# Performance work log

Hardware: AMD Instinct MI355X
Metric: run time of the kernel (lower is better)

Reference implementation:

```python
import jax, jax.numpy as jnp
import numpy as np

CHANNEL = 64
RATIO = 8
C1 = CHANNEL // RATIO


def setup_inputs() -> dict:
    key = jax.random.key(0)
    ks = jax.random.split(key, 8)
    b, c, h, w = 2, CHANNEL, 96, 96
    X = jax.random.normal(ks[0], (b, c, h, w), dtype=jnp.float32)
    Y = jax.random.normal(ks[1], (b, c, h, w), dtype=jnp.float32)
    # 1x1 conv weights (stored as [out, in]) + biases, Kaiming-ish scale
    s = 1.0 / np.sqrt(c)
    Wq = jax.random.uniform(ks[2], (C1, c), jnp.float32, -s, s)
    bq = jax.random.uniform(ks[3], (C1,), jnp.float32, -s, s)
    Wk = jax.random.uniform(ks[4], (C1, c), jnp.float32, -s, s)
    bk = jax.random.uniform(ks[5], (C1,), jnp.float32, -s, s)
    Wv = jax.random.uniform(ks[6], (c, c), jnp.float32, -s, s)
    bv = jax.random.uniform(ks[7], (c,), jnp.float32, -s, s)
    return {"X": X, "Y": Y, "Wq": Wq, "bq": bq, "Wk": Wk, "bk": bk, "Wv": Wv, "bv": bv}


def reference(X, Y, Wq, bq, Wk, bk, Wv, bv):
    b, c, h, w = Y.shape
    n = h * w
    # 1x1 convs as channel contractions -> [b, n, c_out]
    Xf = X.reshape(b, c, n)                       # [b, c, n]
    q = jnp.einsum('oc,bcn->bno', Wq, Xf) + bq    # [b, n, c1]
    k = jnp.einsum('oc,bcn->bno', Wk, Xf) + bk    # [b, n, c1]
    v = jnp.einsum('oc,bcn->bno', Wv, Y.reshape(b, c, n)) + bv  # [b, n, c]
    scores = jnp.einsum('bic,bjc->bij', q, k)     # [b, n, n]
    # NOTE: softmax over dim=1 (the first n axis), as in the original module
    a = jax.nn.softmax(scores, axis=1)
    x = jnp.einsum('bij,bjc->bic', a, v)          # [b, n, c]
    x = x.transpose(0, 2, 1).reshape(b, c, h, w)
    return Y + x
```

## Files before the change

### kernel.cpp

```cpp
#include <hip/hip_runtime.h>

#define NPOS 9216
#define NB 2
#define CCH 64
#define JSPLIT 8
#define JCHUNK (NPOS / JSPLIT)
#define NSTEP (JCHUNK / 64)

typedef __attribute__((ext_vector_type(8))) short short8;
typedef __attribute__((ext_vector_type(4))) short short4b;
typedef __attribute__((ext_vector_type(4))) float f32x4;
typedef __attribute__((ext_vector_type(16))) float f32x16;

#define LOG2E 1.4426950408889634f

__device__ __forceinline__ f32x4 mfma16(short4b a, short4b b, f32x4 c) {
#if defined(__HIP_DEVICE_COMPILE__)
    return __builtin_amdgcn_mfma_f32_16x16x16bf16_1k(a, b, c, 0, 0, 0);
#else
    return c;
#endif
}

__device__ __forceinline__ ushort f2bf(float x) {
    unsigned u = __builtin_bit_cast(unsigned, x);
    u += 0x7FFFu + ((u >> 16) & 1u);
    return (ushort)(u >> 16);
}

__device__ __forceinline__ unsigned cvt_pk_bf16(float lo, float hi) {
    unsigned r;
    asm("v_cvt_pk_bf16_f32 %0, %1, %2" : "=v"(r) : "v"(lo), "v"(hi));
    return r;
}

__global__ __launch_bounds__(256) void qkv_kernel(
    const float* __restrict__ X, const float* __restrict__ Y,
    const float* __restrict__ Wq, const float* __restrict__ bq,
    const float* __restrict__ Wk, const float* __restrict__ bk,
    const float* __restrict__ Wv, const float* __restrict__ bv,
    ushort* __restrict__ qb, ushort* __restrict__ kb,
    ushort* __restrict__ vT, float* __restrict__ out)
{
    __shared__ float wqkT[1024];
    __shared__ float wvTs[4096];
    int tid = threadIdx.x;
    for (int idx = tid; idx < 1024; idx += 256) {
        int c = idx >> 4, o = idx & 15;
        wqkT[idx] = (o < 8) ? Wq[o * 64 + c] : Wk[(o - 8) * 64 + c];
    }
    for (int idx = tid; idx < 4096; idx += 256) {
        int c = idx >> 6, o = idx & 63;
        wvTs[idx] = Wv[o * 64 + c];
    }
    __syncthreads();

    int p = tid & 31, s = tid >> 5;
    int base = blockIdx.x * 32;
    int b = base / NPOS;
    int n = (base % NPOS) + p;

    float va[8], qk[8], ysave[8];
    #pragma unroll
    for (int o = 0; o < 8; ++o) va[o] = bv[s * 8 + o];
    #pragma unroll
    for (int o = 0; o < 8; ++o) qk[o] = 0.f;
    if (s == 0) {
        #pragma unroll
        for (int o = 0; o < 8; ++o) qk[o] = bq[o];
    } else if (s == 1) {
        #pragma unroll
        for (int o = 0; o < 8; ++o) qk[o] = bk[o];
    }

    const float* Xb = X + (size_t)b * CCH * NPOS + n;
    const float* Yb = Y + (size_t)b * CCH * NPOS + n;
    for (int co = 0; co < 8; ++co) {
        #pragma unroll
        for (int ci = 0; ci < 8; ++ci) {
            int c = co * 8 + ci;
            float yv = Yb[(size_t)c * NPOS];
            if (co == s) ysave[ci] = yv;
            const float* wv = wvTs + c * 64 + s * 8;
            #pragma unroll
            for (int o = 0; o < 8; ++o) va[o] += wv[o] * yv;
            if (s < 2) {
                float xv = Xb[(size_t)c * NPOS];
                const float* wq = wqkT + c * 16 + s * 8;
                #pragma unroll
                for (int o = 0; o < 8; ++o) qk[o] += wq[o] * xv;
            }
        }
    }

    ushort* vdst = vT + (size_t)b * CCH * NPOS + n;
    float* ob = out + (size_t)b * CCH * NPOS + n;
    #pragma unroll
    for (int o = 0; o < 8; ++o) {
        vdst[(size_t)(s * 8 + o) * NPOS] = f2bf(va[o]);
        ob[(size_t)(s * 8 + o) * NPOS] = ysave[o];
    }
    if (s < 2) {
        if (s == 0) {
            #pragma unroll
            for (int o = 0; o < 8; ++o) qk[o] *= LOG2E;
        }
        short8 row;
        #pragma unroll
        for (int o = 0; o < 8; ++o) row[o] = (short)f2bf(qk[o]);
        ushort* dst = (s == 0 ? qb : kb) + ((size_t)b * NPOS + n) * 8;
        *(short8*)dst = row;
    }
}

__global__ __launch_bounds__(256) void zpass_kernel(
    const ushort* __restrict__ qb, const ushort* __restrict__ kb,
    float* __restrict__ Z)
{
    int tid = threadIdx.x;
    int w = tid >> 6, l = tid & 63;
    int il2 = l & 31, h = l >> 5;
    int b = blockIdx.z;
    int jb = blockIdx.x * 128 + w * 32;
    int i0 = blockIdx.y * 1152;
    const short8 zero8 = {0,0,0,0,0,0,0,0};
    f32x16 cz16;
    #pragma unroll
    for (int r = 0; r < 16; ++r) cz16[r] = 0.f;

    short8 kf = zero8;
    if (h == 0) kf = *(const short8*)(kb + ((size_t)b * NPOS + jb + il2) * 8);

    f32x16 za = cz16;
    const ushort* qrow = qb + ((size_t)b * NPOS + i0 + il2) * 8;
    short8 qf = (h == 0) ? *(const short8*)qrow : zero8;
    for (int it = 0; it < 36; ++it) {
        short8 qn = zero8;
        if (h == 0 && (it + 1) < 36)
            qn = *(const short8*)(qrow + (size_t)(it + 1) * 256);
        f32x16 sv = __builtin_amdgcn_mfma_f32_32x32x16_bf16(kf, qf, cz16, 0, 0, 0);
        #pragma unroll
        for (int r = 0; r < 16; ++r) za[r] += __builtin_amdgcn_exp2f(sv[r]);
        qf = qn;
    }
    #pragma unroll
    for (int r = 0; r < 16; ++r) {
        float x = za[r];
        x += __shfl_xor(x, 1, 32);
        x += __shfl_xor(x, 2, 32);
        x += __shfl_xor(x, 4, 32);
        x += __shfl_xor(x, 8, 32);
        x += __shfl_xor(x, 16, 32);
        za[r] = x;
    }
    if (il2 == 0) {
        #pragma unroll
        for (int r = 0; r < 16; ++r) {
            int j = jb + (r & 3) + 8 * (r >> 2) + 4 * h;
            atomicAdd(&Z[(size_t)b * NPOS + j], za[r]);
        }
    }
}

__global__ __launch_bounds__(256) void pass2_kernel(
    const ushort* __restrict__ qb, const ushort* __restrict__ kb,
    const ushort* __restrict__ vT, const float* __restrict__ Z,
    float* __restrict__ out)
{
    __shared__ ushort vz[2][64 * 64];
    int tid = threadIdx.x;
    int w = tid >> 6, l = tid & 63;
    int il = l & 15, g = l >> 4;
    int b = blockIdx.z;
    int ibase = blockIdx.x * 64;
    int j0 = blockIdx.y * JCHUNK;
    int jw = w * 16;

    const short8 zero8 = {0,0,0,0,0,0,0,0};
    const f32x4 cz = {0.f,0.f,0.f,0.f};

    short8 qf[4];
    #pragma unroll
    for (int it = 0; it < 4; ++it) {
        qf[it] = zero8;
        if (g == 0)
            qf[it] = *(const short8*)(qb + ((size_t)b * NPOS + ibase + it * 16 + il) * 8);
    }

    f32x4 acc[4][4];
    #pragma unroll
    for (int cg = 0; cg < 4; ++cg)
        #pragma unroll
        for (int it = 0; it < 4; ++it) acc[cg][it] = cz;

    const ushort* kbb = kb + (size_t)b * NPOS * 8;
    const float* Zb = Z + (size_t)b * NPOS;

    int sr = tid >> 2, sq = tid & 3;
    const ushort* vrow = vT + (size_t)b * CCH * NPOS + (size_t)sr * NPOS + j0;
    int so0 = (sq ^ (sr & 7)) * 8;
    int so1 = ((sq + 4) ^ (sr & 7)) * 8;

    {
        float4 ga = *(const float4*)(vrow + sq * 8);
        float4 gb = *(const float4*)(vrow + sq * 8 + 32);
        *(float4*)&vz[0][sr * 64 + so0] = ga;
        *(float4*)&vz[0][sr * 64 + so1] = gb;
    }
    short8 kf = zero8;
    if (g == 0) kf = *(const short8*)(kbb + (size_t)(j0 + jw + il) * 8);
    float4 Zv = *(const float4*)(Zb + j0 + jw + 4 * g);
    __syncthreads();

    int rslot = 2 * w + (g >> 1);
    int rbyte = (g & 1) * 4;

    for (int st = 0; st < NSTEP; ++st) {
        int cur = st & 1;
        bool more = (st + 1) < NSTEP;

        float4 ga = {0,0,0,0}, gb = {0,0,0,0}, Zn = {0,0,0,0};
        short8 kn = zero8;
        if (more) {
            int jn = (st + 1) * 64;
            ga = *(const float4*)(vrow + jn + sq * 8);
            gb = *(const float4*)(vrow + jn + sq * 8 + 32);
            if (g == 0) kn = *(const short8*)(kbb + (size_t)(j0 + jn + jw + il) * 8);
            Zn = *(const float4*)(Zb + j0 + jn + jw + 4 * g);
        }

        f32x4 sv[4];
        #pragma unroll
        for (int it = 0; it < 4; ++it)
            sv[it] = __builtin_amdgcn_mfma_f32_16x16x32_bf16(kf, qf[it], cz, 0, 0, 0);

        float r0 = __builtin_amdgcn_rcpf(Zv.x);
        float r1 = __builtin_amdgcn_rcpf(Zv.y);
        float r2 = __builtin_amdgcn_rcpf(Zv.z);
        float r3 = __builtin_amdgcn_rcpf(Zv.w);

        short4b pf[4];
        #pragma unroll
        for (int it = 0; it < 4; ++it) {
            float p0 = __builtin_amdgcn_exp2f(sv[it][0]) * r0;
            float p1 = __builtin_amdgcn_exp2f(sv[it][1]) * r1;
            float p2 = __builtin_amdgcn_exp2f(sv[it][2]) * r2;
            float p3 = __builtin_amdgcn_exp2f(sv[it][3]) * r3;
            uint2 u;
            u.x = cvt_pk_bf16(p0, p1);
            u.y = cvt_pk_bf16(p2, p3);
            pf[it] = __builtin_bit_cast(short4b, u);
        }

        #pragma unroll
        for (int cg = 0; cg < 4; ++cg) {
            int row = cg * 16 + il;
            short4b af = *(short4b*)&vz[cur][row * 64 + ((rslot ^ (row & 7)) * 8) + rbyte];
            #pragma unroll
            for (int it = 0; it < 4; ++it)
                acc[cg][it] = mfma16(af, pf[it], acc[cg][it]);
        }

        if (more) {
            *(float4*)&vz[cur ^ 1][sr * 64 + so0] = ga;
            *(float4*)&vz[cur ^ 1][sr * 64 + so1] = gb;
            kf = kn; Zv = Zn;
        }
        __syncthreads();
    }

    float* red = (float*)vz;
    float* obase = out + (size_t)b * CCH * NPOS + ibase;
    int i_l = tid >> 2, c0 = (tid & 3) * 4;
    #pragma unroll
    for (int cg = 0; cg < 4; ++cg) {
        #pragma unroll
        for (int it = 0; it < 4; ++it)
            *(f32x4*)&red[w * 1024 + (it * 16 + il) * 16 + 4 * g] = acc[cg][it];
        __syncthreads();
        f32x4 sum = *(f32x4*)&red[tid * 4];
        sum += *(f32x4*)&red[1024 + tid * 4];
        sum += *(f32x4*)&red[2048 + tid * 4];
        sum += *(f32x4*)&red[3072 + tid * 4];
        #pragma unroll
        for (int e = 0; e < 4; ++e)
            atomicAdd(obase + (size_t)(cg * 16 + c0 + e) * NPOS + i_l, sum[e]);
        __syncthreads();
    }
}

extern "C" void kernel_launch(void* const* d_in, const int* in_sizes, int n_in,
                              void* d_out, int out_size, void* d_ws, size_t ws_size,
                              hipStream_t stream) {
    const float* X  = (const float*)d_in[0];
    const float* Y  = (const float*)d_in[1];
    const float* Wq = (const float*)d_in[2];
    const float* bq = (const float*)d_in[3];
    const float* Wk = (const float*)d_in[4];
    const float* bk = (const float*)d_in[5];
    const float* Wv = (const float*)d_in[6];
    const float* bv = (const float*)d_in[7];

    char* ws = (char*)d_ws;
    ushort* qb  = (ushort*)(ws);
    ushort* kbw = (ushort*)(ws + 294912);
    ushort* vT  = (ushort*)(ws + 589824);
    float*  Z   = (float*) (ws + 2949120);

    (void)hipMemsetAsync(Z, 0, (size_t)NB * NPOS * sizeof(float), stream);

    qkv_kernel<<<576, 256, 0, stream>>>(X, Y, Wq, bq, Wk, bk, Wv, bv,
                                        qb, kbw, vT, (float*)d_out);
    zpass_kernel<<<dim3(72, 8, NB), 256, 0, stream>>>(qb, kbw, Z);
    pass2_kernel<<<dim3(144, JSPLIT, NB), 256, 0, stream>>>(qb, kbw, vT, Z,
                                                            (float*)d_out);
}
```

Measured before the change: 199.2 us.

## Replace atomic split-j accumulation with two partial buffers and a combine kernel

Reduces the key-dimension split from 8 to 2. Each pass2 block now writes its partial output with coalesced float4 stores into a workspace buffer instead of doing atomicAdd into the output. A new combine kernel adds Y and the two partials, and qkv no longer writes Y into out. The V shared-memory fill mapping and the reduction buffer padding also change. This removes heavy atomic traffic, at the cost of fewer, longer blocks, an extra kernel launch and extra memory traffic.

```diff
diff --git a/kernel.cpp b/kernel.cpp
--- a/kernel.cpp
+++ b/kernel.cpp
@@ -3,9 +3,10 @@
 #define NPOS 9216
 #define NB 2
 #define CCH 64
-#define JSPLIT 8
+#define JSPLIT 2
 #define JCHUNK (NPOS / JSPLIT)
 #define NSTEP (JCHUNK / 64)
+#define PART_STRIDE ((size_t)NB * CCH * NPOS)
 
 typedef __attribute__((ext_vector_type(8))) short short8;
 typedef __attribute__((ext_vector_type(4))) short short4b;
@@ -40,7 +41,7 @@
     const float* __restrict__ Wk, const float* __restrict__ bk,
     const float* __restrict__ Wv, const float* __restrict__ bv,
     ushort* __restrict__ qb, ushort* __restrict__ kb,
-    ushort* __restrict__ vT, float* __restrict__ out)
+    ushort* __restrict__ vT)
 {
     __shared__ float wqkT[1024];
     __shared__ float wvTs[4096];
@@ -60,7 +61,7 @@
     int b = base / NPOS;
     int n = (base % NPOS) + p;
 
-    float va[8], qk[8], ysave[8];
+    float va[8], qk[8];
     #pragma unroll
     for (int o = 0; o < 8; ++o) va[o] = bv[s * 8 + o];
     #pragma unroll
@@ -75,31 +76,29 @@
 
     const float* Xb = X + (size_t)b * CCH * NPOS + n;
     const float* Yb = Y + (size_t)b * CCH * NPOS + n;
-    for (int co = 0; co < 8; ++co) {
-        #pragma unroll
-        for (int ci = 0; ci < 8; ++ci) {
-            int c = co * 8 + ci;
-            float yv = Yb[(size_t)c * NPOS];
-            if (co == s) ysave[ci] = yv;
-            const float* wv = wvTs + c * 64 + s * 8;
-            #pragma unroll
-            for (int o = 0; o < 8; ++o) va[o] += wv[o] * yv;
-            if (s < 2) {
-                float xv = Xb[(size_t)c * NPOS];
-                const float* wq = wqkT + c * 16 + s * 8;
-                #pragma unroll
-                for (int o = 0; o < 8; ++o) qk[o] += wq[o] * xv;
-            }
+    for (int c = 0; c < 64; ++c) {
+        float yv = Yb[(size_t)c * NPOS];
+        const float4* wv4 = (const float4*)(wvTs + c * 64 + s * 8);
+        float4 w0 = wv4[0], w1 = wv4[1];
+        va[0] += w0.x * yv; va[1] += w0.y * yv;
+        va[2] += w0.z * yv; va[3] += w0.w * yv;
+        va[4] += w1.x * yv; va[5] += w1.y * yv;
+        va[6] += w1.z * yv; va[7] += w1.w * yv;
+        if (s < 2) {
+            float xv = Xb[(size_t)c * NPOS];
+            const float4* wq4 = (const float4*)(wqkT + c * 16 + s * 8);
+            float4 q0 = wq4[0], q1 = wq4[1];
+            qk[0] += q0.x * xv; qk[1] += q0.y * xv;
+            qk[2] += q0.z * xv; qk[3] += q0.w * xv;
+            qk[4] += q1.x * xv; qk[5] += q1.y * xv;
+            qk[6] += q1.z * xv; qk[7] += q1.w * xv;
         }
     }
 
     ushort* vdst = vT + (size_t)b * CCH * NPOS + n;
-    float* ob = out + (size_t)b * CCH * NPOS + n;
-    #pragma unroll
-    for (int o = 0; o < 8; ++o) {
+    #pragma unroll
+    for (int o = 0; o < 8; ++o)
         vdst[(size_t)(s * 8 + o) * NPOS] = f2bf(va[o]);
-        ob[(size_t)(s * 8 + o) * NPOS] = ysave[o];
-    }
     if (s < 2) {
         if (s == 0) {
             #pragma unroll
@@ -165,15 +164,17 @@
 __global__ __launch_bounds__(256) void pass2_kernel(
     const ushort* __restrict__ qb, const ushort* __restrict__ kb,
     const ushort* __restrict__ vT, const float* __restrict__ Z,
-    float* __restrict__ out)
+    float* __restrict__ part)
 {
     __shared__ ushort vz[2][64 * 64];
+    __shared__ float red[4 * 1280];
     int tid = threadIdx.x;
     int w = tid >> 6, l = tid & 63;
     int il = l & 15, g = l >> 4;
     int b = blockIdx.z;
+    int jh = blockIdx.y;
     int ibase = blockIdx.x * 64;
-    int j0 = blockIdx.y * JCHUNK;
+    int j0 = jh * JCHUNK;
     int jw = w * 16;
 
     const short8 zero8 = {0,0,0,0,0,0,0,0};
@@ -196,16 +197,19 @@
     const ushort* kbb = kb + (size_t)b * NPOS * 8;
     const float* Zb = Z + (size_t)b * NPOS;
 
-    int sr = tid >> 2, sq = tid & 3;
-    const ushort* vrow = vT + (size_t)b * CCH * NPOS + (size_t)sr * NPOS + j0;
-    int so0 = (sq ^ (sr & 7)) * 8;
-    int so1 = ((sq + 4) ^ (sr & 7)) * 8;
+    int r0 = w * 16 + (l >> 3);
+    int sl = l & 7;
+    int jq = sl ^ (r0 & 7);
+    const ushort* vsrc0 = vT + (size_t)b * CCH * NPOS + (size_t)r0 * NPOS + j0 + jq * 8;
+    const ushort* vsrc1 = vsrc0 + (size_t)8 * NPOS;
+    int wo0 = r0 * 64 + sl * 8;
+    int wo1 = wo0 + 8 * 64;
 
     {
-        float4 ga = *(const float4*)(vrow + sq * 8);
-        float4 gb = *(const float4*)(vrow + sq * 8 + 32);
-        *(float4*)&vz[0][sr * 64 + so0] = ga;
-        *(float4*)&vz[0][sr * 64 + so1] = gb;
+        float4 ga = *(const float4*)vsrc0;
+        float4 gb = *(const float4*)vsrc1;
+        *(float4*)&vz[0][wo0] = ga;
+        *(float4*)&vz[0][wo1] = gb;
     }
     short8 kf = zero8;
     if (g == 0) kf = *(const short8*)(kbb + (size_t)(j0 + jw + il) * 8);
@@ -223,8 +227,8 @@
         short8 kn = zero8;
         if (more) {
             int jn = (st + 1) * 64;
-            ga = *(const float4*)(vrow + jn + sq * 8);
-            gb = *(const float4*)(vrow + jn + sq * 8 + 32);
+            ga = *(const float4*)(vsrc0 + jn);
+            gb = *(const float4*)(vsrc1 + jn);
             if (g == 0) kn = *(const short8*)(kbb + (size_t)(j0 + jn + jw + il) * 8);
             Zn = *(const float4*)(Zb + j0 + jn + jw + 4 * g);
         }
@@ -234,18 +238,18 @@
         for (int it = 0; it < 4; ++it)
             sv[it] = __builtin_amdgcn_mfma_f32_16x16x32_bf16(kf, qf[it], cz, 0, 0, 0);
 
-        float r0 = __builtin_amdgcn_rcpf(Zv.x);
-        float r1 = __builtin_amdgcn_rcpf(Zv.y);
-        float r2 = __builtin_amdgcn_rcpf(Zv.z);
-        float r3 = __builtin_amdgcn_rcpf(Zv.w);
+        float rz0 = __builtin_amdgcn_rcpf(Zv.x);
+        float rz1 = __builtin_amdgcn_rcpf(Zv.y);
+        float rz2 = __builtin_amdgcn_rcpf(Zv.z);
+        float rz3 = __builtin_amdgcn_rcpf(Zv.w);
 
         short4b pf[4];
         #pragma unroll
         for (int it = 0; it < 4; ++it) {
-            float p0 = __builtin_amdgcn_exp2f(sv[it][0]) * r0;
-            float p1 = __builtin_amdgcn_exp2f(sv[it][1]) * r1;
-            float p2 = __builtin_amdgcn_exp2f(sv[it][2]) * r2;
-            float p3 = __builtin_amdgcn_exp2f(sv[it][3]) * r3;
+            float p0 = __builtin_amdgcn_exp2f(sv[it][0]) * rz0;
+            float p1 = __builtin_amdgcn_exp2f(sv[it][1]) * rz1;
+            float p2 = __builtin_amdgcn_exp2f(sv[it][2]) * rz2;
+            float p3 = __builtin_amdgcn_exp2f(sv[it][3]) * rz3;
             uint2 u;
             u.x = cvt_pk_bf16(p0, p1);
             u.y = cvt_pk_bf16(p2, p3);
@@ -262,31 +266,47 @@
         }
 
         if (more) {
-            *(float4*)&vz[cur ^ 1][sr * 64 + so0] = ga;
-            *(float4*)&vz[cur ^ 1][sr * 64 + so1] = gb;
+            *(float4*)&vz[cur ^ 1][wo0] = ga;
+            *(float4*)&vz[cur ^ 1][wo1] = gb;
             kf = kn; Zv = Zn;
         }
         __syncthreads();
     }
 
-    float* red = (float*)vz;
-    float* obase = out + (size_t)b * CCH * NPOS + ibase;
-    int i_l = tid >> 2, c0 = (tid & 3) * 4;
+    float* pbase = part + (size_t)jh * PART_STRIDE + (size_t)b * CCH * NPOS + ibase;
+    int c_l = tid >> 4, i0 = (tid & 15) * 4;
     #pragma unroll
     for (int cg = 0; cg < 4; ++cg) {
         #pragma unroll
         for (int it = 0; it < 4; ++it)
-            *(f32x4*)&red[w * 1024 + (it * 16 + il) * 16 + 4 * g] = acc[cg][it];
+            *(f32x4*)&red[w * 1280 + (it * 16 + il) * 20 + 4 * g] = acc[cg][it];
         __syncthreads();
-        f32x4 sum = *(f32x4*)&red[tid * 4];
-        sum += *(f32x4*)&red[1024 + tid * 4];
-        sum += *(f32x4*)&red[2048 + tid * 4];
-        sum += *(f32x4*)&red[3072 + tid * 4];
-        #pragma unroll
-        for (int e = 0; e < 4; ++e)
-            atomicAdd(obase + (size_t)(cg * 16 + c0 + e) * NPOS + i_l, sum[e]);
+        float4 sum;
+        float* sp = (float*)&sum;
+        #pragma unroll
+        for (int d = 0; d < 4; ++d) {
+            int o = (i0 + d) * 20 + c_l;
+            sp[d] = red[o] + red[1280 + o] + red[2560 + o] + red[3840 + o];
+        }
+        *(float4*)&pbase[(size_t)(cg * 16 + c_l) * NPOS + i0] = sum;
         __syncthreads();
     }
+}
+
+__global__ __launch_bounds__(256) void combine_kernel(
+    const float* __restrict__ Y, const float* __restrict__ part,
+    float* __restrict__ out)
+{
+    size_t idx = ((size_t)blockIdx.x * 256 + threadIdx.x) * 4;
+    float4 y = *(const float4*)(Y + idx);
+    float4 a = *(const float4*)(part + idx);
+    float4 c = *(const float4*)(part + PART_STRIDE + idx);
+    float4 o;
+    o.x = y.x + a.x + c.x;
+    o.y = y.y + a.y + c.y;
+    o.z = y.z + a.z + c.z;
+    o.w = y.w + a.w + c.w;
+    *(float4*)(out + idx) = o;
 }
 
 extern "C" void kernel_launch(void* const* d_in, const int* in_sizes, int n_in,
@@ -302,16 +322,17 @@
     const float* bv = (const float*)d_in[7];
 
     char* ws = (char*)d_ws;
-    ushort* qb  = (ushort*)(ws);
-    ushort* kbw = (ushort*)(ws + 294912);
-    ushort* vT  = (ushort*)(ws + 589824);
-    float*  Z   = (float*) (ws + 2949120);
+    ushort* qb   = (ushort*)(ws);
+    ushort* kbw  = (ushort*)(ws + 294912);
+    ushort* vT   = (ushort*)(ws + 589824);
+    float*  Z    = (float*) (ws + 2949120);
+    float*  part = (float*) (ws + 3022848);
 
     (void)hipMemsetAsync(Z, 0, (size_t)NB * NPOS * sizeof(float), stream);
 
     qkv_kernel<<<576, 256, 0, stream>>>(X, Y, Wq, bq, Wk, bk, Wv, bv,
-                                        qb, kbw, vT, (float*)d_out);
+                                        qb, kbw, vT);
     zpass_kernel<<<dim3(72, 8, NB), 256, 0, stream>>>(qb, kbw, Z);
-    pass2_kernel<<<dim3(144, JSPLIT, NB), 256, 0, stream>>>(qb, kbw, vT, Z,
-                                                            (float*)d_out);
-}
+    pass2_kernel<<<dim3(144, JSPLIT, NB), 256, 0, stream>>>(qb, kbw, vT, Z, part);
+    combine_kernel<<<1152, 256, 0, stream>>>(Y, part, (float*)d_out);
+}
```

Result: slower. 207.5 us (+4.2%).
